# Kernel optimization log

Measured on AMD Instinct MI355X. Metric: run time of the kernel, lower is better.

The kernel has to match this reference:

```python
import jax, jax.numpy as jnp
import numpy as np

H = 5  # LSTM hidden size


def _lstm_layer(x, Wih, Whh, bih, bhh):
    # x: [B, T, D]; Wih: [4H, D]; Whh: [4H, H]; biases: [4H]
    B, T, _ = x.shape
    # precompute input contribution with one big GEMM (torch gate order i,f,g,o)
    xg = jnp.einsum('btd,gd->btg', x, Wih) + bih + bhh  # [B,T,4H]
    xg = jnp.swapaxes(xg, 0, 1)  # [T,B,4H]
    WhhT = Whh.T

    def step(carry, g_t):
        h, c = carry
        g = g_t + h @ WhhT
        i, f, gg, o = jnp.split(g, 4, axis=-1)
        i = jax.nn.sigmoid(i)
        f = jax.nn.sigmoid(f)
        gg = jnp.tanh(gg)
        o = jax.nn.sigmoid(o)
        c = f * c + i * gg
        h = o * jnp.tanh(c)
        return (h, c), h

    h0 = jnp.zeros((B, H), x.dtype)
    c0 = jnp.zeros((B, H), x.dtype)
    _, hs = jax.lax.scan(step, (h0, c0), xg)
    return jnp.swapaxes(hs, 0, 1)  # [B,T,H]


def _stacked_lstm(x, params):
    for (Wih, Whh, bih, bhh) in params:
        x = _lstm_layer(x, Wih, Whh, bih, bhh)
    return x


def setup_inputs() -> dict:
    key = jax.random.key(0)
    ks = jax.random.split(key, 24)
    B, T, D = 512, 1024, 225
    s = 1.0 / np.sqrt(H)

    def u(k, shape):
        return jax.random.uniform(k, shape, jnp.float32, -s, s)

    inp = {"x": jax.random.normal(ks[0], (B, T, D), jnp.float32)}
    # lstm1: layer0 input D=225, layer1 input H=5
    inp["l1_Wih0"] = u(ks[1], (4 * H, D)); inp["l1_Whh0"] = u(ks[2], (4 * H, H))
    inp["l1_bih0"] = u(ks[3], (4 * H,)); inp["l1_bhh0"] = u(ks[4], (4 * H,))
    inp["l1_Wih1"] = u(ks[5], (4 * H, H)); inp["l1_Whh1"] = u(ks[6], (4 * H, H))
    inp["l1_bih1"] = u(ks[7], (4 * H,)); inp["l1_bhh1"] = u(ks[8], (4 * H,))
    inp["fc1_W"] = u(ks[9], (H, H)); inp["fc1_b"] = u(ks[10], (H,))
    # lstm2: both layers input H=5
    inp["l2_Wih0"] = u(ks[11], (4 * H, H)); inp["l2_Whh0"] = u(ks[12], (4 * H, H))
    inp["l2_bih0"] = u(ks[13], (4 * H,)); inp["l2_bhh0"] = u(ks[14], (4 * H,))
    inp["l2_Wih1"] = u(ks[15], (4 * H, H)); inp["l2_Whh1"] = u(ks[16], (4 * H, H))
    inp["l2_bih1"] = u(ks[17], (4 * H,)); inp["l2_bhh1"] = u(ks[18], (4 * H,))
    inp["fc2_W"] = u(ks[19], (H, H)); inp["fc2_b"] = u(ks[20], (H,))
    return inp


def reference(x, l1_Wih0, l1_Whh0, l1_bih0, l1_bhh0,
              l1_Wih1, l1_Whh1, l1_bih1, l1_bhh1,
              fc1_W, fc1_b,
              l2_Wih0, l2_Whh0, l2_bih0, l2_bhh0,
              l2_Wih1, l2_Whh1, l2_bih1, l2_bhh1,
              fc2_W, fc2_b):
    # dropout layers are identity in inference mode
    h = _stacked_lstm(x, [(l1_Wih0, l1_Whh0, l1_bih0, l1_bhh0),
                          (l1_Wih1, l1_Whh1, l1_bih1, l1_bhh1)])
    h = jax.nn.relu(h @ fc1_W.T + fc1_b)
    h = _stacked_lstm(h, [(l2_Wih0, l2_Whh0, l2_bih0, l2_bhh0),
                          (l2_Wih1, l2_Whh1, l2_bih1, l2_bhh1)])
    return jax.nn.sigmoid(h @ fc2_W.T + fc2_b)
```

## Files before the change

kernel.cpp:

```cpp
#include <hip/hip_runtime.h>
#include <math.h>

#define T_STEPS 1024
#define B_SIZE  512
#define D_IN    225
#define WT_K    228
#define LOG2E   1.4426950408889634f

typedef float f32x2 __attribute__((ext_vector_type(2)));

__device__ __forceinline__ float fexp2(float x) {
#if __has_builtin(__builtin_amdgcn_exp2f)
  return __builtin_amdgcn_exp2f(x);
#else
  return exp2f(x);
#endif
}
__device__ __forceinline__ float frcp(float x) {
#if __has_builtin(__builtin_amdgcn_rcpf)
  return __builtin_amdgcn_rcpf(x);
#else
  return 1.0f / x;
#endif
}
#define SIG(x) frcp(1.0f + fexp2((x) * (-LOG2E)))
#define TH(x)  fmaf(2.0f, frcp(1.0f + fexp2((x) * (-2.0f * LOG2E))), -1.0f)

#define GL16(gp, lp) __builtin_amdgcn_global_load_lds(                          \
    (const __attribute__((address_space(1))) void*)(gp),                        \
    (__attribute__((address_space(3))) void*)(lp), 16, 0, 0)
#define GL4(gp, lp)  __builtin_amdgcn_global_load_lds(                          \
    (const __attribute__((address_space(1))) void*)(gp),                        \
    (__attribute__((address_space(3))) void*)(lp), 4, 0, 0)

#define WAIT_VM0() do {                                                         \
    asm volatile("s_waitcnt vmcnt(0)" ::: "memory");                            \
    __builtin_amdgcn_sched_barrier(0);                                          \
  } while (0)
#define WAIT_VM10() do {                                                        \
    asm volatile("s_waitcnt vmcnt(10)" ::: "memory");                           \
    __builtin_amdgcn_sched_barrier(0);                                          \
  } while (0)

__global__ __launch_bounds__(256)
void prep_wt(const float* __restrict__ Wih, const float* __restrict__ bih,
             const float* __restrict__ bhh, float* __restrict__ wt2)
{
  int i = blockIdx.x * 256 + threadIdx.x;
  int g = i / WT_K, kk = i - g * WT_K;
  float v = 0.f;
  if (g < 20 && kk < 225) v = Wih[g * 225 + kk];
  if (i >= 4560 && i < 4580) v = bih[i - 4560] + bhh[i - 4560];
  wt2[i] = v;
}

__global__ __launch_bounds__(256)
void xg_gemm(const float* __restrict__ x, const float* __restrict__ wtg,
             float* __restrict__ xg)
{
  __shared__ __align__(16) float xsA[64 * 116];
  __shared__ __align__(16) float xsB[64 * 112];
  __shared__ __align__(16) float wt[4608];
  __shared__ float xs224[64];
  const int tid  = threadIdx.x;
  const int lane = tid & 63;
  const int w    = __builtin_amdgcn_readfirstlane(tid >> 6);

  const uint32_t base = (uint32_t)blockIdx.x * 57600u;

  for (int m = w; m < 18; m += 4)
    GL16(wtg + m * 256 + lane * 4, wt + m * 256);
  for (int m = w; m < 29; m += 4) {
    uint32_t c = (uint32_t)(m * 64 + lane);
    uint32_t r = __umulhi(c, 148102321u);
    uint32_t q = c - 29u * r;
    GL16((const char*)x + base + r * 900u + q * 16u, (char*)xsA + m * 1024);
  }
  __syncthreads();

  for (int m = w; m < 28; m += 4) {
    uint32_t c = (uint32_t)(m * 64 + lane);
    uint32_t r = __umulhi(c, 153391690u);
    uint32_t q = c - 28u * r;
    GL16((const char*)x + base + r * 900u + 448u + q * 16u, (char*)xsB + m * 1024);
  }
  if (w == 0)
    GL4(x + (size_t)blockIdx.x * 14400 + lane * 225 + 224, xs224 + lane);

  const float* wr = wt + (5 * w) * WT_K;
  float acc[5];
#pragma unroll
  for (int j = 0; j < 5; ++j) acc[j] = wt[4560 + 5 * w + j];

  {
    const float* xr = xsA + lane * 116;
#pragma unroll 7
    for (int kb = 0; kb < 112; kb += 4) {
      const float4 xv = *(const float4*)(xr + kb);
#pragma unroll
      for (int j = 0; j < 5; ++j) {
        const float4 wv = *(const float4*)(wr + j * WT_K + kb);
        acc[j] = fmaf(xv.x, wv.x, acc[j]);
        acc[j] = fmaf(xv.y, wv.y, acc[j]);
        acc[j] = fmaf(xv.z, wv.z, acc[j]);
        acc[j] = fmaf(xv.w, wv.w, acc[j]);
      }
    }
  }
  __syncthreads();

  {
    const float* xr = xsB + lane * 112;
#pragma unroll 7
    for (int kb = 0; kb < 112; kb += 4) {
      const float4 xv = *(const float4*)(xr + kb);
#pragma unroll
      for (int j = 0; j < 5; ++j) {
        const float4 wv = *(const float4*)(wr + j * WT_K + 112 + kb);
        acc[j] = fmaf(xv.x, wv.x, acc[j]);
        acc[j] = fmaf(xv.y, wv.y, acc[j]);
        acc[j] = fmaf(xv.z, wv.z, acc[j]);
        acc[j] = fmaf(xv.w, wv.w, acc[j]);
      }
    }
    float xl = xs224[lane];
#pragma unroll
    for (int j = 0; j < 5; ++j) acc[j] = fmaf(xl, wr[j * WT_K + 224], acc[j]);
  }
  float* op = xg + ((size_t)blockIdx.x * 64 + lane) * 20 + w;
#pragma unroll
  for (int j = 0; j < 5; ++j) op[4 * j] = acc[j];
}

__global__ __launch_bounds__(64)
void lstm_fused(const float* __restrict__ xg, float* __restrict__ out,
              const float* __restrict__ l1_Whh0,
              const float* __restrict__ l1_Wih1, const float* __restrict__ l1_Whh1,
              const float* __restrict__ l1_bih1, const float* __restrict__ l1_bhh1,
              const float* __restrict__ fc1_W,  const float* __restrict__ fc1_b,
              const float* __restrict__ l2_Wih0, const float* __restrict__ l2_Whh0,
              const float* __restrict__ l2_bih0, const float* __restrict__ l2_bhh0,
              const float* __restrict__ l2_Wih1, const float* __restrict__ l2_Whh1,
              const float* __restrict__ l2_bih1, const float* __restrict__ l2_bhh1,
              const float* __restrict__ fc2_W,  const float* __restrict__ fc2_b)
{
  __shared__ __align__(16) float xq[2][2][1280];
  __shared__ float outb[2][64][5];
  const int lane  = threadIdx.x & 63;
  const int half  = lane >> 5;
  const int l32   = lane & 31;
  const int stage = (l32 < 30) ? (l32 / 5) : 6;
  const int u     = (l32 < 30) ? (l32 - stage * 5) : 0;
  const int b0    = blockIdx.x * 2;

  const bool is_l0   = (stage == 0);
  const bool is_relu = (stage == 2);
  const bool is_fc   = (stage == 2) || (stage == 5);
  const bool is_fc2  = (stage == 5);

  float wi[4][5] = {}, wh[4][5] = {}, bs[4] = {};
  if (stage == 0) {
#pragma unroll
    for (int q = 0; q < 4; ++q)
#pragma unroll
      for (int j = 0; j < 5; ++j) wh[q][j] = l1_Whh0[(u + 5 * q) * 5 + j];
  } else if (stage == 1) {
#pragma unroll
    for (int q = 0; q < 4; ++q) {
#pragma unroll
      for (int j = 0; j < 5; ++j) {
        wi[q][j] = l1_Wih1[(u + 5 * q) * 5 + j];
        wh[q][j] = l1_Whh1[(u + 5 * q) * 5 + j];
      }
      bs[q] = l1_bih1[u + 5 * q] + l1_bhh1[u + 5 * q];
    }
  } else if (stage == 3) {
#pragma unroll
    for (int q = 0; q < 4; ++q) {
#pragma unroll
      for (int j = 0; j < 5; ++j) {
        wi[q][j] = l2_Wih0[(u + 5 * q) * 5 + j];
        wh[q][j] = l2_Whh0[(u + 5 * q) * 5 + j];
      }
      bs[q] = l2_bih0[u + 5 * q] + l2_bhh0[u + 5 * q];
    }
  } else if (stage == 4) {
#pragma unroll
    for (int q = 0; q < 4; ++q) {
#pragma unroll
      for (int j = 0; j < 5; ++j) {
        wi[q][j] = l2_Wih1[(u + 5 * q) * 5 + j];
        wh[q][j] = l2_Whh1[(u + 5 * q) * 5 + j];
      }
      bs[q] = l2_bih1[u + 5 * q] + l2_bhh1[u + 5 * q];
    }
  } else if (stage == 2) {
#pragma unroll
    for (int j = 0; j < 5; ++j) wi[0][j] = fc1_W[u * 5 + j];
    bs[0] = fc1_b[u];
  } else if (stage == 5) {
#pragma unroll
    for (int j = 0; j < 5; ++j) wi[0][j] = fc2_W[u * 5 + j];
    bs[0] = fc2_b[u];
  }

  f32x2 wi01[5], wi23[5], wh01[5], wh23[5];
#pragma unroll
  for (int j = 0; j < 5; ++j) {
    wi01[j] = f32x2{wi[0][j], wi[1][j]};
    wi23[j] = f32x2{wi[2][j], wi[3][j]};
    wh01[j] = f32x2{wh[0][j], wh[1][j]};
    wh23[j] = f32x2{wh[2][j], wh[3][j]};
  }
  const f32x2 bs01 = f32x2{bs[0], bs[1]};
  const f32x2 bs23 = f32x2{bs[2], bs[3]};

  int ii[5], ih[5];
  const int bse = half * 32;
  const int inb = (stage >= 1 && stage <= 5) ? (stage - 1) * 5 : 0;
  const int hb_ = (stage <= 5) ? stage * 5 : 0;
#pragma unroll
  for (int j = 0; j < 5; ++j) {
    ii[j] = (bse + inb + j) * 4;
    ih[j] = (bse + hb_ + j) * 4;
  }

  const float* obf = &outb[0][0][0];
  float* outbase = out + (size_t)b0 * T_STEPS * 5;
  int lof[10], ofs[10];
  bool fg1[10], fg2[10];
#pragma unroll
  for (int i2 = 0; i2 < 10; ++i2) {
    int idx = i2 * 64 + lane;
    int e  = (idx >= 320) ? 1 : 0;
    int r  = idx - e * 320;
    int tq = r / 5;
    int j2 = r - tq * 5;
    lof[i2] = e * 320 + (((tq - 5) & 63) * 5) + j2;
    ofs[i2] = e * (T_STEPS * 5) + tq * 5 + j2;
    fg1[i2] = (tq >= 5);
    fg2[i2] = (tq < 5);
  }

  const float* src0 = xg + (size_t)(b0 + 0) * T_STEPS * 20;
  const float* src1 = xg + (size_t)(b0 + 1) * T_STEPS * 20;

#define STAGE_CHUNK(CH, BUF)                                                   \
  { const float* s0_ = src0 + (CH) * 1280;                                     \
    const float* s1_ = src1 + (CH) * 1280;                                     \
    float* d0_ = &xq[BUF][0][0];                                               \
    float* d1_ = &xq[BUF][1][0];                                               \
    _Pragma("unroll")                                                          \
    for (int m = 0; m < 5; ++m) {                                              \
      GL16(s0_ + m * 256 + lane * 4, d0_ + m * 256);                           \
      GL16(s1_ + m * 256 + lane * 4, d1_ + m * 256);                           \
    } }

#define TICK(QV, GUARDED, KVAL)                                                \
  { const int hvi_ = __float_as_int(hv);                                       \
    float inx[5], hhx[5];                                                      \
    _Pragma("unroll")                                                          \
    for (int j = 0; j < 5; ++j) {                                              \
      inx[j] = __int_as_float(__builtin_amdgcn_ds_bpermute(ii[j], hvi_));      \
      hhx[j] = __int_as_float(__builtin_amdgcn_ds_bpermute(ih[j], hvi_));      \
    }                                                                          \
    f32x2 a01 = is_l0 ? f32x2{(QV).x, (QV).y} : bs01;                          \
    f32x2 a23 = is_l0 ? f32x2{(QV).z, (QV).w} : bs23;                          \
    f32x2 b01, b23;                                                            \
    { const f32x2 h0 = f32x2{hhx[0], hhx[0]};                                  \
      b01 = wh01[0] * h0; b23 = wh23[0] * h0; }                                \
    _Pragma("unroll")                                                          \
    for (int j = 0; j < 5; ++j) {                                              \
      const f32x2 xj = f32x2{inx[j], inx[j]};                                  \
      a01 = __builtin_elementwise_fma(wi01[j], xj, a01);                       \
      a23 = __builtin_elementwise_fma(wi23[j], xj, a23);                       \
    }                                                                          \
    _Pragma("unroll")                                                          \
    for (int j = 1; j < 5; ++j) {                                              \
      const f32x2 hj = f32x2{hhx[j], hhx[j]};                                  \
      b01 = __builtin_elementwise_fma(wh01[j], hj, b01);                       \
      b23 = __builtin_elementwise_fma(wh23[j], hj, b23);                       \
    }                                                                          \
    const f32x2 pre01 = a01 + b01, pre23 = a23 + b23;                          \
    float i_ = SIG(pre01.x), f_ = SIG(pre01.y);                                \
    float g_ = TH(pre23.x),  o_ = SIG(pre23.y);                                \
    float cn = fmaf(f_, c, i_ * g_);                                           \
    float hl = o_ * TH(cn);                                                    \
    float fx = is_relu ? fmaxf(pre01.x, 0.0f) : i_;                            \
    float hn = is_fc ? fx : hl;                                                \
    if (GUARDED) { bool ok = (KVAL) >= stage; c = ok ? cn : c; hv = ok ? hn : hv; } \
    else         { c = cn; hv = hn; }                                          \
    if (is_fc2) outb[half][((KVAL) + 59) & 63][u] = i_;                        \
  }

#define LQ(T) (*(const float4*)(xqb + 20 * (T)))
#define MINQ(X) (((X) > 63) ? 63 : (X))

#define CHUNK_BODY(GUARDED)                                                    \
  { float4 qA = LQ(0), qB = LQ(1), qC = LQ(2), qD = LQ(3);                     \
    _Pragma("unroll")                                                          \
    for (int g4 = 0; g4 < 16; ++g4) {                                          \
      const int kk = g4 * 4;                                                   \
      TICK(qA, GUARDED, kk + 0)                                                \
      qA = LQ(MINQ(kk + 4));                                                   \
      TICK(qB, GUARDED, kk + 1)                                                \
      qB = LQ(MINQ(kk + 5));                                                   \
      TICK(qC, GUARDED, kk + 2)                                                \
      qC = LQ(MINQ(kk + 6));                                                   \
      TICK(qD, GUARDED, kk + 3)                                                \
      qD = LQ(MINQ(kk + 7));                                                   \
    } }

#define FLUSH(TBASE, MODE)                                                     \
  { _Pragma("unroll")                                                          \
    for (int i2 = 0; i2 < 10; ++i2) {                                          \
      float v = obf[lof[i2]];                                                  \
      bool ok = (MODE == 0) || ((MODE == 1) ? fg1[i2] : fg2[i2]);              \
      if (ok) outbase[ofs[i2] + (TBASE) * 5] = v;                              \
    } }

  float hv = 0.f, c = 0.f;

  STAGE_CHUNK(0, 0)
  WAIT_VM0();

  {
    STAGE_CHUNK(1, 1)
    const float* xqb = &xq[0][half][4 * u];
    CHUNK_BODY(true)
    FLUSH(-5, 1)
    WAIT_VM10();
  }
  for (int ch = 1; ch < 16; ++ch) {
    if (ch < 15) STAGE_CHUNK(ch + 1, (ch + 1) & 1)
    const float* xqb = &xq[ch & 1][half][4 * u];
    CHUNK_BODY(false)
    FLUSH(ch * 64 - 5, 0)
    WAIT_VM10();
  }
  {
    const float* xqb = &xq[0][half][4 * u];
    float4 qZ = LQ(0);
    TICK(qZ, false, 0)
    TICK(qZ, false, 1)
    TICK(qZ, false, 2)
    TICK(qZ, false, 3)
    TICK(qZ, false, 4)
    FLUSH(T_STEPS - 5, 2)
  }

#undef STAGE_CHUNK
#undef TICK
#undef LQ
#undef MINQ
#undef CHUNK_BODY
#undef FLUSH
}

extern "C" void kernel_launch(void* const* d_in, const int* in_sizes, int n_in,
                              void* d_out, int out_size, void* d_ws, size_t ws_size,
                              hipStream_t stream)
{
  const float* x        = (const float*)d_in[0];
  const float* l1_Wih0  = (const float*)d_in[1];
  const float* l1_Whh0  = (const float*)d_in[2];
  const float* l1_bih0  = (const float*)d_in[3];
  const float* l1_bhh0  = (const float*)d_in[4];
  const float* l1_Wih1  = (const float*)d_in[5];
  const float* l1_Whh1  = (const float*)d_in[6];
  const float* l1_bih1  = (const float*)d_in[7];
  const float* l1_bhh1  = (const float*)d_in[8];
  const float* fc1_W    = (const float*)d_in[9];
  const float* fc1_b    = (const float*)d_in[10];
  const float* l2_Wih0  = (const float*)d_in[11];
  const float* l2_Whh0  = (const float*)d_in[12];
  const float* l2_bih0  = (const float*)d_in[13];
  const float* l2_bhh0  = (const float*)d_in[14];
  const float* l2_Wih1  = (const float*)d_in[15];
  const float* l2_Whh1  = (const float*)d_in[16];
  const float* l2_bih1  = (const float*)d_in[17];
  const float* l2_bhh1  = (const float*)d_in[18];
  const float* fc2_W    = (const float*)d_in[19];
  const float* fc2_b    = (const float*)d_in[20];

  float* xg   = (float*)d_ws;
  float* wtws = xg + 10485760;
  float* out  = (float*)d_out;

  prep_wt<<<dim3(18), dim3(256), 0, stream>>>(l1_Wih0, l1_bih0, l1_bhh0, wtws);

  xg_gemm<<<dim3((B_SIZE * T_STEPS) / 64), dim3(256), 0, stream>>>(x, wtws, xg);

  lstm_fused<<<dim3(B_SIZE / 2), dim3(64), 0, stream>>>(
      xg, out, l1_Whh0, l1_Wih1, l1_Whh1, l1_bih1, l1_bhh1,
      fc1_W, fc1_b, l2_Wih0, l2_Whh0, l2_bih0, l2_bhh0,
      l2_Wih1, l2_Whh1, l2_bih1, l2_bhh1, fc2_W, fc2_b);
}
```

Before: 389.6 us.

## Make xg_gemm persistent over 16 tiles with double-buffered LDS prefetch

The input-projection GEMM kernel now launches 512 blocks, each looping over 16 row tiles instead of one block per tile. The weight tile is loaded into LDS once per block, and the next tile's first half is prefetched while the second half is computed, using explicit vmcnt waits and barriers. This is meant to cut launch and per-block weight-reload overhead and to overlap global-to-LDS loads with FMA work. The hand-counted vmcnt values make correctness fragile, and fewer blocks may reduce the number of loads in flight across the GPU.

```diff
diff --git a/kernel.cpp b/kernel.cpp
--- a/kernel.cpp
+++ b/kernel.cpp
@@ -39,6 +39,10 @@
   } while (0)
 #define WAIT_VM10() do {                                                        \
     asm volatile("s_waitcnt vmcnt(10)" ::: "memory");                           \
+    __builtin_amdgcn_sched_barrier(0);                                          \
+  } while (0)
+#define BARRIER_VM(N) do {                                                      \
+    asm volatile("s_waitcnt vmcnt(" #N ")\n\ts_barrier" ::: "memory");          \
     __builtin_amdgcn_sched_barrier(0);                                          \
   } while (0)
 
@@ -58,78 +62,103 @@
 void xg_gemm(const float* __restrict__ x, const float* __restrict__ wtg,
              float* __restrict__ xg)
 {
-  __shared__ __align__(16) float xsA[64 * 116];
-  __shared__ __align__(16) float xsB[64 * 112];
+  __shared__ __align__(16) float xsA[8192];
+  __shared__ __align__(16) float xsB[7168];
   __shared__ __align__(16) float wt[4608];
   __shared__ float xs224[64];
   const int tid  = threadIdx.x;
   const int lane = tid & 63;
   const int w    = __builtin_amdgcn_readfirstlane(tid >> 6);
 
-  const uint32_t base = (uint32_t)blockIdx.x * 57600u;
+  const int tile0 = blockIdx.x * 16;
+
+#define ISSUE_A(TI)                                                            \
+  { const uint32_t base_ = (uint32_t)(TI) * 57600u;                            \
+    _Pragma("unroll")                                                          \
+    for (int i_ = 0; i_ < 8; ++i_) {                                           \
+      int m_ = w * 8 + i_;                                                     \
+      uint32_t c_ = (uint32_t)(m_ * 64 + lane);                                \
+      c_ = (c_ > 1855u) ? 1855u : c_;            \
+      uint32_t r_ = __umulhi(c_, 148102321u);                      \
+      uint32_t q_ = c_ - 29u * r_;                                             \
+      GL16((const char*)x + base_ + r_ * 900u + q_ * 16u,                      \
+           (char*)xsA + m_ * 1024);                                            \
+    } }
+
+#define ISSUE_B(TI)                                                            \
+  { const uint32_t base_ = (uint32_t)(TI) * 57600u;                            \
+    _Pragma("unroll")                                                          \
+    for (int i_ = 0; i_ < 7; ++i_) {                                           \
+      int m_ = w * 7 + i_;                                                     \
+      uint32_t c_ = (uint32_t)(m_ * 64 + lane);                                \
+      uint32_t r_ = __umulhi(c_, 153391690u);                      \
+      uint32_t q_ = c_ - 28u * r_;                                             \
+      GL16((const char*)x + base_ + r_ * 900u + 448u + q_ * 16u,               \
+           (char*)xsB + m_ * 1024);                                            \
+    }                                                                          \
+    GL4(x + (size_t)(TI) * 14400 + lane * 225 + 224, xs224 + lane); }
 
   for (int m = w; m < 18; m += 4)
     GL16(wtg + m * 256 + lane * 4, wt + m * 256);
-  for (int m = w; m < 29; m += 4) {
-    uint32_t c = (uint32_t)(m * 64 + lane);
-    uint32_t r = __umulhi(c, 148102321u);
-    uint32_t q = c - 29u * r;
-    GL16((const char*)x + base + r * 900u + q * 16u, (char*)xsA + m * 1024);
-  }
-  __syncthreads();
-
-  for (int m = w; m < 28; m += 4) {
-    uint32_t c = (uint32_t)(m * 64 + lane);
-    uint32_t r = __umulhi(c, 153391690u);
-    uint32_t q = c - 28u * r;
-    GL16((const char*)x + base + r * 900u + 448u + q * 16u, (char*)xsB + m * 1024);
-  }
-  if (w == 0)
-    GL4(x + (size_t)blockIdx.x * 14400 + lane * 225 + 224, xs224 + lane);
+  ISSUE_A(tile0)
+  WAIT_VM0();
+  __builtin_amdgcn_s_barrier();
 
   const float* wr = wt + (5 * w) * WT_K;
-  float acc[5];
-#pragma unroll
-  for (int j = 0; j < 5; ++j) acc[j] = wt[4560 + 5 * w + j];
-
-  {
-    const float* xr = xsA + lane * 116;
+
+  for (int t = 0; t < 16; ++t) {
+    const int tile = tile0 + t;
+    ISSUE_B(tile)
+
+    float acc[5];
+#pragma unroll
+    for (int j = 0; j < 5; ++j) acc[j] = wt[4560 + 5 * w + j];
+
+    {
+      const float* xr = xsA + lane * 116;
 #pragma unroll 7
-    for (int kb = 0; kb < 112; kb += 4) {
-      const float4 xv = *(const float4*)(xr + kb);
-#pragma unroll
-      for (int j = 0; j < 5; ++j) {
-        const float4 wv = *(const float4*)(wr + j * WT_K + kb);
-        acc[j] = fmaf(xv.x, wv.x, acc[j]);
-        acc[j] = fmaf(xv.y, wv.y, acc[j]);
-        acc[j] = fmaf(xv.z, wv.z, acc[j]);
-        acc[j] = fmaf(xv.w, wv.w, acc[j]);
+      for (int kb = 0; kb < 112; kb += 4) {
+        const float4 xv = *(const float4*)(xr + kb);
+#pragma unroll
+        for (int j = 0; j < 5; ++j) {
+          const float4 wv = *(const float4*)(wr + j * WT_K + kb);
+          acc[j] = fmaf(xv.x, wv.x, acc[j]);
+          acc[j] = fmaf(xv.y, wv.y, acc[j]);
+          acc[j] = fmaf(xv.z, wv.z, acc[j]);
+          acc[j] = fmaf(xv.w, wv.w, acc[j]);
+        }
       }
     }
-  }
-  __syncthreads();
-
-  {
-    const float* xr = xsB + lane * 112;
+    BARRIER_VM(0);
+
+    if (t < 15) ISSUE_A(tile + 1)
+
+    {
+      const float* xr = xsB + lane * 112;
 #pragma unroll 7
-    for (int kb = 0; kb < 112; kb += 4) {
-      const float4 xv = *(const float4*)(xr + kb);
-#pragma unroll
-      for (int j = 0; j < 5; ++j) {
-        const float4 wv = *(const float4*)(wr + j * WT_K + 112 + kb);
-        acc[j] = fmaf(xv.x, wv.x, acc[j]);
-        acc[j] = fmaf(xv.y, wv.y, acc[j]);
-        acc[j] = fmaf(xv.z, wv.z, acc[j]);
-        acc[j] = fmaf(xv.w, wv.w, acc[j]);
+      for (int kb = 0; kb < 112; kb += 4) {
+        const float4 xv = *(const float4*)(xr + kb);
+#pragma unroll
+        for (int j = 0; j < 5; ++j) {
+          const float4 wv = *(const float4*)(wr + j * WT_K + 112 + kb);
+          acc[j] = fmaf(xv.x, wv.x, acc[j]);
+          acc[j] = fmaf(xv.y, wv.y, acc[j]);
+          acc[j] = fmaf(xv.z, wv.z, acc[j]);
+          acc[j] = fmaf(xv.w, wv.w, acc[j]);
+        }
       }
+      float xl = xs224[lane];
+#pragma unroll
+      for (int j = 0; j < 5; ++j) acc[j] = fmaf(xl, wr[j * WT_K + 224], acc[j]);
     }
-    float xl = xs224[lane];
-#pragma unroll
-    for (int j = 0; j < 5; ++j) acc[j] = fmaf(xl, wr[j * WT_K + 224], acc[j]);
-  }
-  float* op = xg + ((size_t)blockIdx.x * 64 + lane) * 20 + w;
-#pragma unroll
-  for (int j = 0; j < 5; ++j) op[4 * j] = acc[j];
+    float* op = xg + ((size_t)tile * 64 + lane) * 20 + w;
+#pragma unroll
+    for (int j = 0; j < 5; ++j) op[4 * j] = acc[j];
+
+    BARRIER_VM(5);
+  }
+#undef ISSUE_A
+#undef ISSUE_B
 }
 
 __global__ __launch_bounds__(64)
@@ -389,7 +418,7 @@
 
   prep_wt<<<dim3(18), dim3(256), 0, stream>>>(l1_Wih0, l1_bih0, l1_bhh0, wtws);
 
-  xg_gemm<<<dim3((B_SIZE * T_STEPS) / 64), dim3(256), 0, stream>>>(x, wtws, xg);
+  xg_gemm<<<dim3(512), dim3(256), 0, stream>>>(x, wtws, xg);
 
   lstm_fused<<<dim3(B_SIZE / 2), dim3(64), 0, stream>>>(
       xg, out, l1_Whh0, l1_Wih1, l1_Whh1, l1_bih1, l1_bhh1,
```

New measurement: 429.0 us. 10.1% more time.
